# Kernel tuning notes

Measured on AMD Instinct MI355X. Metric: run time of the kernel, lower is better.

The kernel has to match this reference:

```python
import jax, jax.numpy as jnp
import numpy as np

B, M, K, KNN = 2, 256, 64, 16
CXYZ, CFEAT = 3, 61
CIN = CXYZ + CFEAT  # 64
MLPS = [64, 128]
SUMM = sum(MLPS)    # 192
CALIB = 64
EXP = [256, 512]
OUT = 256
EPS = 1e-5


def bn(x, g, b):
    # BatchNorm eval mode with running_mean=0, running_var=1 (channel axis 1)
    shape = (1, -1) + (1,) * (x.ndim - 2)
    return x * (g / jnp.sqrt(1.0 + EPS)).reshape(shape) + b.reshape(shape)


def knn(x, k):
    xx = jnp.sum(x * x, axis=1)                      # (B, N)
    inner = jnp.einsum('bcn,bcm->bnm', x, x)         # (B, N, N)
    pd = 2.0 * inner - xx[:, :, None] - xx[:, None, :]
    return jax.lax.top_k(pd, k)[1]                   # (B, N, k)


def graph_feature(x, idx):
    # x: (B, C, N), idx: (B, N, k) -> (B, 2C, N, k)
    xt = jnp.transpose(x, (0, 2, 1))                 # (B, N, C)
    nb = jax.vmap(lambda a, i: a[i])(xt, idx)        # (B, N, k, C)
    ctr = xt[:, :, None, :]
    feat = jnp.concatenate([nb - ctr, jnp.broadcast_to(ctr, nb.shape)], axis=-1)
    return jnp.transpose(feat, (0, 3, 1, 2))


def forward(xyz, feats, e1_w, e1_g, e1_b, e2_w, e2_g, e2_b,
            cal1_w, cal1_g, cal1_b, cal2_w, cal2_bias,
            exp1_w, exp1_g, exp1_b, exp2_w, exp2_g, exp2_b,
            red_w, red_g, red_b, sc1_w, sc1_b, sc2_w, sc2_b,
            sc_n1_g, sc_n1_b, sc_n2_g, sc_n2_b):
    x3 = xyz.reshape(B * M, K, CXYZ).transpose(0, 2, 1)      # (BM, 3, K)
    f = feats.reshape(B * M, K, CFEAT).transpose(0, 2, 1)    # (BM, 61, K)
    idx = knn(x3, KNN)                                        # USE_FEATS_DIS=False: knn once on xyz
    x = jnp.concatenate([x3, f], axis=1)                      # (BM, 64, K)
    outs = []
    for W, g, b in ((e1_w, e1_g, e1_b), (e2_w, e2_g, e2_b)):
        gf = graph_feature(x, idx)                            # (BM, 2C, K, knn)
        y = jax.nn.relu(bn(jnp.einsum('oc,bcnk->bonk', W, gf), g, b))
        x = y.max(axis=-1)                                    # (BM, mlp_i, K)
        outs.append(x)
    x = jnp.concatenate(outs, axis=1)                         # (BM, 192, K)
    c = jax.nn.relu(bn(jnp.einsum('oc,bcn->bon', cal1_w, x), cal1_g, cal1_b))
    c = jnp.einsum('oc,bcn->bon', cal2_w, c) + cal2_bias[None, :, None]
    x = jax.nn.sigmoid(c) * x
    x = jax.nn.relu(bn(jnp.einsum('oc,bcn->bon', exp1_w, x), exp1_g, exp1_b))
    x = jax.nn.relu(bn(jnp.einsum('oc,bcn->bon', exp2_w, x), exp2_g, exp2_b))
    x = x.max(axis=-1).reshape(B, M, EXP[1]).transpose(0, 2, 1)  # (B, 512, M)
    x = jax.nn.relu(bn(jnp.einsum('oc,bcm->bom', red_w, x), red_g, red_b))
    x = bn(x + x, sc_n1_g, sc_n1_b)
    h = jax.nn.relu(jnp.einsum('oc,bcm->bom', sc1_w, x) + sc1_b[None, :, None])
    h = jnp.einsum('oc,bcm->bom', sc2_w, h) + sc2_b[None, :, None]
    x = bn(x + h, sc_n2_g, sc_n2_b)
    return x                                                  # (B, 256, M)


def setup_inputs() -> dict:
    key = jax.random.key(0)
    ks = jax.random.split(key, 16)
    w = lambda k, s: jax.random.normal(k, s, jnp.float32) * 0.05
    ones = lambda n: jnp.ones((n,), jnp.float32)
    zeros = lambda n: jnp.zeros((n,), jnp.float32)
    return {
        'xyz': jax.random.normal(ks[0], (B, M, K, CXYZ), jnp.float32),
        'feats': jax.random.normal(ks[1], (B, M, K, CFEAT), jnp.float32),
        'e1_w': w(ks[2], (MLPS[0], 2 * CIN)), 'e1_g': ones(MLPS[0]), 'e1_b': zeros(MLPS[0]),
        'e2_w': w(ks[3], (MLPS[1], 2 * MLPS[0])), 'e2_g': ones(MLPS[1]), 'e2_b': zeros(MLPS[1]),
        'cal1_w': w(ks[4], (CALIB, SUMM)), 'cal1_g': ones(CALIB), 'cal1_b': zeros(CALIB),
        'cal2_w': w(ks[5], (SUMM, CALIB)), 'cal2_bias': zeros(SUMM),
        'exp1_w': w(ks[6], (EXP[0], SUMM)), 'exp1_g': ones(EXP[0]), 'exp1_b': zeros(EXP[0]),
        'exp2_w': w(ks[7], (EXP[1], EXP[0])), 'exp2_g': ones(EXP[1]), 'exp2_b': zeros(EXP[1]),
        'red_w': w(ks[8], (OUT, EXP[1])), 'red_g': ones(OUT), 'red_b': zeros(OUT),
        'sc1_w': w(ks[9], (OUT, OUT)), 'sc1_b': zeros(OUT),
        'sc2_w': w(ks[10], (OUT, OUT)), 'sc2_b': zeros(OUT),
        'sc_n1_g': ones(OUT), 'sc_n1_b': zeros(OUT),
        'sc_n2_g': ones(OUT), 'sc_n2_b': zeros(OUT),
    }


def reference(xyz, feats, e1_w, e1_g, e1_b, e2_w, e2_g, e2_b,
              cal1_w, cal1_g, cal1_b, cal2_w, cal2_bias,
              exp1_w, exp1_g, exp1_b, exp2_w, exp2_g, exp2_b,
              red_w, red_g, red_b, sc1_w, sc1_b, sc2_w, sc2_b,
              sc_n1_g, sc_n1_b, sc_n2_g, sc_n2_b):
    return forward(xyz, feats, e1_w, e1_g, e1_b, e2_w, e2_g, e2_b,
                   cal1_w, cal1_g, cal1_b, cal2_w, cal2_bias,
                   exp1_w, exp1_g, exp1_b, exp2_w, exp2_g, exp2_b,
                   red_w, red_g, red_b, sc1_w, sc1_b, sc2_w, sc2_b,
                   sc_n1_g, sc_n1_b, sc_n2_g, sc_n2_b)
```

## Files before the change

### kernel.cpp

```cpp
#include <hip/hip_runtime.h>
#include <hip/hip_bf16.h>
#include <math.h>
#include <stddef.h>

#define DEV __device__ __forceinline__
__device__ const float BNS = 0.99999500003749968f;

typedef __bf16 bf16x8 __attribute__((ext_vector_type(8)));
typedef float  f32x4  __attribute__((ext_vector_type(4)));

#define MF(a,b,c) __builtin_amdgcn_mfma_f32_16x16x32_bf16(a,b,c,0,0,0)

DEV unsigned short f2bs(float v){
  union{ __hip_bfloat16 b; unsigned short u; } c; c.b=__float2bfloat16(v); return c.u;
}
DEV float bs2f(unsigned short u){
  union{ unsigned short u; __hip_bfloat16 b; } c; c.u=u; return __bfloat162float(c.b);
}

DEV void put_split4(unsigned short* chunks, int n, int c0, const float* v){
  int cc=c0>>5, u=(c0>>3)&3, e=c0&7;
  unsigned short* base = chunks + cc*4096;
  unsigned short h0=f2bs(v[0]), h1=f2bs(v[1]), h2=f2bs(v[2]), h3=f2bs(v[3]);
  ushort4 hq = make_ushort4(h0,h1,h2,h3);
  ushort4 lq = make_ushort4(f2bs(v[0]-bs2f(h0)), f2bs(v[1]-bs2f(h1)),
                            f2bs(v[2]-bs2f(h2)), f2bs(v[3]-bs2f(h3)));
  *(ushort4*)&base[(n*8 + (u     ^ (n&7)))*8 + e] = hq;
  *(ushort4*)&base[(n*8 + ((u+4) ^ (n&7)))*8 + e] = lq;
}
DEV void get_split4(const unsigned short* chunks, int n, int c0, float* v){
  int cc=c0>>5, u=(c0>>3)&3, e=c0&7;
  const unsigned short* base = chunks + cc*4096;
  ushort4 hq = *(const ushort4*)&base[(n*8 + (u     ^ (n&7)))*8 + e];
  ushort4 lq = *(const ushort4*)&base[(n*8 + ((u+4) ^ (n&7)))*8 + e];
  v[0]=bs2f(hq.x)+bs2f(lq.x); v[1]=bs2f(hq.y)+bs2f(lq.y);
  v[2]=bs2f(hq.z)+bs2f(lq.z); v[3]=bs2f(hq.w)+bs2f(lq.w);
}


__global__ __launch_bounds__(256) void k_prep(const float* __restrict__ e1_w,
    const float* __restrict__ e2_w, const float* __restrict__ cal1_w,
    const float* __restrict__ cal2_w, const float* __restrict__ exp1_w,
    const float* __restrict__ exp2_w, unsigned short* __restrict__ Whi,
    unsigned short* __restrict__ Wlo,
    const float* __restrict__ red_w, const float* __restrict__ sc1_w,
    const float* __restrict__ sc2_w, float* __restrict__ Wt_red,
    float* __restrict__ Wt_s1, float* __restrict__ Wt_s2){
  __shared__ float s[32][33];
  int bid = blockIdx.x;
  if(bid < 896){
    const float* src; unsigned short *hi,*lo; int mode, O=0, i0;
    if(bid<32)      { src=e1_w;  hi=Whi;       lo=Wlo;       mode=1; O= 64; i0=bid*256; }
    else if(bid<96) { src=e2_w;  hi=Whi+8192;  lo=Wlo+8192;  mode=1; O=128; i0=(bid-32)*256; }
    else if(bid<144){ src=cal1_w;hi=Whi+24576; lo=Wlo+24576; mode=0;        i0=(bid-96)*256; }
    else if(bid<192){ src=cal2_w;hi=Whi+36864; lo=Wlo+36864; mode=0;        i0=(bid-144)*256; }
    else if(bid<384){ src=exp1_w;hi=Whi+49152; lo=Wlo+49152; mode=0;        i0=(bid-192)*256; }
    else            { src=exp2_w;hi=Whi+98304; lo=Wlo+98304; mode=0;        i0=(bid-384)*256; }
    int i = i0 + threadIdx.x;
    float v;
    if(mode==0) v = src[i];
    else {
      int row=i>>6, c=i&63;
      v = (row<O) ? src[row*128+c] : (src[(row-O)*128+64+c]-src[(row-O)*128+c]);
    }
    unsigned short h=f2bs(v); hi[i]=h; lo[i]=f2bs(v-bs2f(h));
  } else {
    int lb = bid-896;
    const float* in; float* out; int O,K;
    if(lb<128){ in=red_w; out=Wt_red; O=256; K=512; }
    else if(lb<192){ in=sc1_w; out=Wt_s1; O=256; K=256; lb-=128; }
    else { in=sc2_w; out=Wt_s2; O=256; K=256; lb-=192; }
    int nt=O>>5;
    int to=lb%nt, tk=lb/nt;
    int c=threadIdx.x&31, r8=threadIdx.x>>5;
    #pragma unroll
    for(int p=0;p<4;p++){
      int r=r8+p*8;
      s[r][c]=in[(size_t)(to*32+r)*K + tk*32 + c];
    }
    __syncthreads();
    #pragma unroll
    for(int p=0;p<4;p++){
      int r=r8+p*8;
      out[(size_t)(tk*32+r)*O + to*32 + c]=s[c][r];
    }
  }
}

__global__ __launch_bounds__(512) void k_knne12(const float* __restrict__ xyz,
    const float* __restrict__ feats,
    const unsigned short* __restrict__ W1h, const unsigned short* __restrict__ W1l,
    const unsigned short* __restrict__ W2h, const unsigned short* __restrict__ W2l,
    const float* __restrict__ g1, const float* __restrict__ b1,
    const float* __restrict__ g2, const float* __restrict__ b2,
    unsigned short* __restrict__ cat){
  __shared__ float bufA[64*65];
  __shared__ float bufB[64*65];
  __shared__ __align__(16) unsigned short sb[64*136];
  __shared__ int   ips[64*16];
  __shared__ float sx0[64], sx1[64], sx2[64], sxx[64];
  int bm = blockIdx.x;
  int tid = threadIdx.x, n = tid&63, s = tid>>6;
  int wid = tid>>6, lane = tid&63;
  int l15 = lane&15, q = lane>>4;
  if(s==0){
    const float* xp = xyz + (size_t)(bm*64+n)*3;
    float px=xp[0], py=xp[1], pz=xp[2];
    sx0[n]=px; sx1[n]=py; sx2[n]=pz; sxx[n]=px*px+py*py+pz*pz;
  }
  __syncthreads();
  {
    int p = lane>>3, seg = lane&7;
    int n1 = wid*8 + p;
    float px=sx0[n1], py=sx1[n1], pz=sx2[n1], xxn=sxx[n1];
    float pdr[8];
    #pragma unroll
    for(int t=0;t<8;t++){
      int m = seg*8+t;
      pdr[t] = 2.f*(px*sx0[m]+py*sx1[m]+pz*sx2[m]) - xxn - sxx[m];
    }
    for(int j=0;j<16;j++){
      float bv=-3.4e38f; int bi=seg*8;
      #pragma unroll
      for(int t=0;t<8;t++){ if(pdr[t]>bv){bv=pdr[t]; bi=seg*8+t;} }
      float ov; int oi;
      ov=__shfl_xor(bv,1); oi=__shfl_xor(bi,1);
      if(ov>bv || (ov==bv && oi<bi)){bv=ov;bi=oi;}
      ov=__shfl_xor(bv,2); oi=__shfl_xor(bi,2);
      if(ov>bv || (ov==bv && oi<bi)){bv=ov;bi=oi;}
      ov=__shfl_xor(bv,4); oi=__shfl_xor(bi,4);
      if(ov>bv || (ov==bv && oi<bi)){bv=ov;bi=oi;}
      if(seg==0) ips[n1*16+j]=bi;
      if((bi>>3)==seg) pdr[bi&7]=-3.4e38f;
    }
  }
  {
    unsigned short* r = sb + n*136;
    if(s==0){
      float px=sx0[n], py=sx1[n], pz=sx2[n];
      unsigned short h;
      h=f2bs(px); r[0]=h; r[64]=f2bs(px-bs2f(h));
      h=f2bs(py); r[1]=h; r[65]=f2bs(py-bs2f(h));
      h=f2bs(pz); r[2]=h; r[66]=f2bs(pz-bs2f(h));
    }
    const float* fp = feats + (size_t)(bm*64+n)*61;
    #pragma unroll
    for(int t=0;t<8;t++){
      int cc = s*8+t;
      if(cc<61){
        float v=fp[cc]; unsigned short h=f2bs(v);
        r[3+cc]=h; r[64+3+cc]=f2bs(v-bs2f(h));
      }
    }
  }
  __syncthreads();
  {
    int rbase = wid*16;
    f32x4 acc[4];
    #pragma unroll
    for(int d=0;d<4;d++) acc[d]=(f32x4){0.f,0.f,0.f,0.f};
    #pragma unroll
    for(int kc=0;kc<2;kc++){
      int k0=kc*32;
      size_t a0=(size_t)(rbase+l15)*64 + k0 + q*8;
      bf16x8 a0h=*(const bf16x8*)(W1h+a0), a0l=*(const bf16x8*)(W1l+a0);
      #pragma unroll
      for(int nt=0;nt<4;nt++){
        int row = nt*16 + l15;
        bf16x8 bh = *(const bf16x8*)&sb[row*136 + k0 + q*8];
        bf16x8 bl = *(const bf16x8*)&sb[row*136 + 64 + k0 + q*8];
        acc[nt]=MF(a0h,bh,acc[nt]);
        acc[nt]=MF(a0h,bl,acc[nt]);
        acc[nt]=MF(a0l,bh,acc[nt]);
      }
    }
    __syncthreads();
    float* dst = (wid<4)? bufA : bufB;
    int ro = (wid&3)*16;
    #pragma unroll
    for(int nt=0;nt<4;nt++)
      #pragma unroll
      for(int rr=0;rr<4;rr++)
        dst[(ro+q*4+rr)*65 + nt*16+l15] = acc[nt][rr];
  }
  __syncthreads();
  {
    int o = lane;
    float sc = g1[o]*BNS, bi = b1[o];
    #pragma unroll 4
    for(int j=0;j<8;j++){
      int nn = wid*8 + j;
      const int* ip = &ips[nn*16];
      float mz = -3.4e38f;
      #pragma unroll
      for(int k=0;k<16;k++) mz = fmaxf(mz, bufA[o*65 + ip[k]]);
      float v = fmaxf(sc*(mz + bufB[o*65 + nn]) + bi, 0.f);
      unsigned short hv = f2bs(v), lv = f2bs(v - bs2f(hv));
      size_t cb = ((size_t)bm*64+nn)*384 + o;
      cat[cb] = hv; cat[cb+192] = lv;
      sb[nn*136 + o] = hv; sb[nn*136 + 64 + o] = lv;
    }
  }
  for(int ch=0; ch<2; ch++){
    __syncthreads();
    int wrow = ((wid<4)?0:128) + ch*64 + (wid&3)*16;
    f32x4 acc[4];
    #pragma unroll
    for(int d=0;d<4;d++) acc[d]=(f32x4){0.f,0.f,0.f,0.f};
    #pragma unroll
    for(int kc=0;kc<2;kc++){
      int k0=kc*32;
      size_t a0=(size_t)(wrow+l15)*64 + k0 + q*8;
      bf16x8 a0h=*(const bf16x8*)(W2h+a0), a0l=*(const bf16x8*)(W2l+a0);
      #pragma unroll
      for(int nt=0;nt<4;nt++){
        int row = nt*16 + l15;
        bf16x8 bh = *(const bf16x8*)&sb[row*136 + k0 + q*8];
        bf16x8 bl = *(const bf16x8*)&sb[row*136 + 64 + k0 + q*8];
        acc[nt]=MF(a0h,bh,acc[nt]);
        acc[nt]=MF(a0h,bl,acc[nt]);
        acc[nt]=MF(a0l,bh,acc[nt]);
      }
    }
    __syncthreads();
    float* dst = (wid<4)? bufA : bufB;
    int ro = (wid&3)*16;
    #pragma unroll
    for(int nt=0;nt<4;nt++)
      #pragma unroll
      for(int rr=0;rr<4;rr++)
        dst[(ro+q*4+rr)*65 + nt*16+l15] = acc[nt][rr];
    __syncthreads();
    int o = ch*64 + lane;
    float sc = g2[o]*BNS, bi = b2[o];
    #pragma unroll 4
    for(int j=0;j<8;j++){
      int nn = wid*8 + j;
      const int* ip = &ips[nn*16];
      float mz = -3.4e38f;
      #pragma unroll
      for(int k=0;k<16;k++) mz = fmaxf(mz, bufA[lane*65 + ip[k]]);
      float v = fmaxf(sc*(mz + bufB[lane*65 + nn]) + bi, 0.f);
      unsigned short hv = f2bs(v);
      size_t cb = ((size_t)bm*64+nn)*384 + 64 + o;
      cat[cb] = hv; cat[cb+192] = f2bs(v - bs2f(hv));
    }
  }
}

__global__ __launch_bounds__(512,4) void k_mlp(
    const unsigned short* __restrict__ Whi, const unsigned short* __restrict__ Wlo,
    const unsigned short* __restrict__ cats,
    const float* __restrict__ c1g, const float* __restrict__ c1b,
    const float* __restrict__ c2bias,
    const float* __restrict__ e1g, const float* __restrict__ e1b,
    const float* __restrict__ e2g, const float* __restrict__ e2b,
    float* __restrict__ pool){
  __shared__ __align__(16) unsigned short buf[8*4096];
  __shared__ __align__(16) unsigned short calB[2*4096];
  int bm = blockIdx.x;
  int tid = threadIdx.x, wid = tid>>6, lane = tid&63;
  int l15 = lane&15, q = lane>>4;

  const unsigned short* w1h = Whi + 24576;
  const unsigned short* w1l = Wlo + 24576;
  int c1ot = wid>>1, c1rh = wid&1;
  size_t c1wo0 = (size_t)(c1ot*16+l15)*192 + q*8;
  bf16x8 cah = *(const bf16x8*)(w1h+c1wo0);
  bf16x8 cal_ = *(const bf16x8*)(w1l+c1wo0);

  size_t xb = (size_t)bm*24576;
  #pragma unroll
  for(int i=0;i<6;i++){
    int U = tid + i*512;
    int kc = U>>9, w = U&511, rr = w>>3, up = w&7, u = up ^ (rr&7);
    const unsigned short* src = cats + xb + (size_t)rr*384
      + (u<4 ? (kc*32 + u*8) : (192 + kc*32 + (u-4)*8));
    *(uint4*)&buf[kc*4096 + w*8] = *(const uint4*)src;
  }
  __syncthreads();

  f32x4 a0={0.f,0.f,0.f,0.f}, a1={0.f,0.f,0.f,0.f};
  {
    int r0 = c1rh*32+l15, r1 = c1rh*32+16+l15;
    __builtin_amdgcn_s_setprio(1);
    #pragma unroll
    for(int kc=0;kc<6;kc++){
      bf16x8 nah, nal;
      if(kc<5){
        size_t wo = c1wo0 + (kc+1)*32;
        nah=*(const bf16x8*)(w1h+wo); nal=*(const bf16x8*)(w1l+wo);
      }
      const unsigned short* cb = buf + kc*4096;
      bf16x8 xh0=*(const bf16x8*)&cb[(r0*8+((  q)^(r0&7)))*8];
      bf16x8 xl0=*(const bf16x8*)&cb[(r0*8+((4+q)^(r0&7)))*8];
      bf16x8 xh1=*(const bf16x8*)&cb[(r1*8+((  q)^(r1&7)))*8];
      bf16x8 xl1=*(const bf16x8*)&cb[(r1*8+((4+q)^(r1&7)))*8];
      a0=MF(cah,xh0,a0); a1=MF(cah,xh1,a1);
      a0=MF(cah,xl0,a0); a1=MF(cah,xl1,a1);
      a0=MF(cal_,xh0,a0); a1=MF(cal_,xh1,a1);
      cah=nah; cal_=nal;
    }
    __builtin_amdgcn_s_setprio(0);
  }
  const unsigned short* w2h = Whi + 36864;
  const unsigned short* w2l = Wlo + 36864;
  bf16x8 c2h[6], c2l[6];
  #pragma unroll
  for(int i=0;i<6;i++){
    int ot = (wid*6+i)>>2;
    size_t wo=(size_t)(ot*16+l15)*64 + q*8;
    c2h[i]=*(const bf16x8*)(w2h+wo); c2l[i]=*(const bf16x8*)(w2l+wo);
  }
  {
    int c0 = c1ot*16+q*4;
    float4 sg = *(const float4*)&c1g[c0];
    float4 bb = *(const float4*)&c1b[c0];
    float v0[4], v1[4];
    v0[0]=fmaxf(a0[0]*sg.x*BNS+bb.x,0.f); v1[0]=fmaxf(a1[0]*sg.x*BNS+bb.x,0.f);
    v0[1]=fmaxf(a0[1]*sg.y*BNS+bb.y,0.f); v1[1]=fmaxf(a1[1]*sg.y*BNS+bb.y,0.f);
    v0[2]=fmaxf(a0[2]*sg.z*BNS+bb.z,0.f); v1[2]=fmaxf(a1[2]*sg.z*BNS+bb.z,0.f);
    v0[3]=fmaxf(a0[3]*sg.w*BNS+bb.w,0.f); v1[3]=fmaxf(a1[3]*sg.w*BNS+bb.w,0.f);
    put_split4(calB, c1rh*32+l15,    c0, v0);
    put_split4(calB, c1rh*32+16+l15, c0, v1);
  }
  __syncthreads();
  f32x4 ac[6];
  #pragma unroll
  for(int i=0;i<6;i++) ac[i]=(f32x4){0.f,0.f,0.f,0.f};
  #pragma unroll
  for(int kc=0;kc<2;kc++){
    const unsigned short* cb = calB + kc*4096;
    if(kc==1){
      #pragma unroll
      for(int i=0;i<6;i++){
        int ot = (wid*6+i)>>2;
        size_t wo=(size_t)(ot*16+l15)*64 + 32 + q*8;
        c2h[i]=*(const bf16x8*)(w2h+wo); c2l[i]=*(const bf16x8*)(w2l+wo);
      }
    }
    __builtin_amdgcn_s_setprio(1);
    #pragma unroll
    for(int i=0;i<6;i++){
      int nf=(wid*6+i)&3;
      int r=nf*16+l15;
      bf16x8 xh=*(const bf16x8*)&cb[(r*8+((  q)^(r&7)))*8];
      bf16x8 xl=*(const bf16x8*)&cb[(r*8+((4+q)^(r&7)))*8];
      ac[i]=MF(c2h[i],xh,ac[i]); ac[i]=MF(c2h[i],xl,ac[i]); ac[i]=MF(c2l[i],xh,ac[i]);
    }
    __builtin_amdgcn_s_setprio(0);
  }
  const unsigned short* e1wh=Whi+49152; const unsigned short* e1wl=Wlo+49152;
  int ob1 = wid*32;
  bf16x8 p1h[2], p1l[2];
  #pragma unroll
  for(int mt=0;mt<2;mt++){
    size_t wo=(size_t)(ob1+mt*16+l15)*192 + q*8;
    p1h[mt]=*(const bf16x8*)(e1wh+wo); p1l[mt]=*(const bf16x8*)(e1wl+wo);
  }
  #pragma unroll
  for(int i=0;i<6;i++){
    int j=wid*6+i, ot=j>>2, nf=j&3, n=nf*16+l15;
    int c0=ot*16+q*4;
    float4 cb4 = *(const float4*)&c2bias[c0];
    float xv[4];
    get_split4(buf, n, c0, xv);
    xv[0] *= 1.f/(1.f+__expf(-(ac[i][0]+cb4.x)));
    xv[1] *= 1.f/(1.f+__expf(-(ac[i][1]+cb4.y)));
    xv[2] *= 1.f/(1.f+__expf(-(ac[i][2]+cb4.z)));
    xv[3] *= 1.f/(1.f+__expf(-(ac[i][3]+cb4.w)));
    put_split4(buf, n, c0, xv);
  }
  __syncthreads();
  {
    f32x4 e1a[2][4];
    #pragma unroll
    for(int a=0;a<2;a++)
      #pragma unroll
      for(int d=0;d<4;d++) e1a[a][d]=(f32x4){0.f,0.f,0.f,0.f};
    __builtin_amdgcn_s_setprio(1);
    #pragma unroll
    for(int kc=0;kc<6;kc++){
      bf16x8 nh[2], nl[2];
      if(kc<5){
        #pragma unroll
        for(int mt=0;mt<2;mt++){
          size_t wo=(size_t)(ob1+mt*16+l15)*192 + (kc+1)*32 + q*8;
          nh[mt]=*(const bf16x8*)(e1wh+wo); nl[mt]=*(const bf16x8*)(e1wl+wo);
        }
      }
      const unsigned short* cb = buf + kc*4096;
      #pragma unroll
      for(int nf=0;nf<4;nf++){
        int r=nf*16+l15;
        bf16x8 xh=*(const bf16x8*)&cb[(r*8+((  q)^(r&7)))*8];
        bf16x8 xl=*(const bf16x8*)&cb[(r*8+((4+q)^(r&7)))*8];
        e1a[0][nf]=MF(p1h[0],xh,e1a[0][nf]); e1a[1][nf]=MF(p1h[1],xh,e1a[1][nf]);
        e1a[0][nf]=MF(p1h[0],xl,e1a[0][nf]); e1a[1][nf]=MF(p1h[1],xl,e1a[1][nf]);
        e1a[0][nf]=MF(p1l[0],xh,e1a[0][nf]); e1a[1][nf]=MF(p1l[1],xh,e1a[1][nf]);
      }
      p1h[0]=nh[0]; p1h[1]=nh[1]; p1l[0]=nl[0]; p1l[1]=nl[1];
    }
    __builtin_amdgcn_s_setprio(0);
    __syncthreads();
    const unsigned short* e2wh=Whi+98304; const unsigned short* e2wl=Wlo+98304;
    int ob2 = wid*64;
    bf16x8 p2h[4], p2l[4];
    #pragma unroll
    for(int mt=0;mt<4;mt++){
      size_t wo=(size_t)(ob2+mt*16+l15)*256 + q*8;
      p2h[mt]=*(const bf16x8*)(e2wh+wo); p2l[mt]=*(const bf16x8*)(e2wl+wo);
    }
    #pragma unroll
    for(int mt=0;mt<2;mt++){
      int c0 = ob1+mt*16+q*4;
      float4 sg = *(const float4*)&e1g[c0];
      float4 bb = *(const float4*)&e1b[c0];
      #pragma unroll
      for(int nf=0;nf<4;nf++){
        float v[4];
        v[0]=fmaxf(e1a[mt][nf][0]*sg.x*BNS+bb.x,0.f);
        v[1]=fmaxf(e1a[mt][nf][1]*sg.y*BNS+bb.y,0.f);
        v[2]=fmaxf(e1a[mt][nf][2]*sg.z*BNS+bb.z,0.f);
        v[3]=fmaxf(e1a[mt][nf][3]*sg.w*BNS+bb.w,0.f);
        put_split4(buf, nf*16+l15, c0, v);
      }
    }
    __syncthreads();
    f32x4 a2[4][4];
    #pragma unroll
    for(int a=0;a<4;a++)
      #pragma unroll
      for(int d=0;d<4;d++) a2[a][d]=(f32x4){0.f,0.f,0.f,0.f};
    {
      const unsigned short* cb = buf;
      __builtin_amdgcn_s_setprio(1);
      #pragma unroll
      for(int nf=0;nf<4;nf++){
        int r=nf*16+l15;
        bf16x8 xh=*(const bf16x8*)&cb[(r*8+((  q)^(r&7)))*8];
        bf16x8 xl=*(const bf16x8*)&cb[(r*8+((4+q)^(r&7)))*8];
        #pragma unroll
        for(int mt=0;mt<4;mt++) a2[mt][nf]=MF(p2h[mt],xh,a2[mt][nf]);
        #pragma unroll
        for(int mt=0;mt<4;mt++) a2[mt][nf]=MF(p2h[mt],xl,a2[mt][nf]);
        #pragma unroll
        for(int mt=0;mt<4;mt++) a2[mt][nf]=MF(p2l[mt],xh,a2[mt][nf]);
      }
      __builtin_amdgcn_s_setprio(0);
    }
    for(int kc=1;kc<8;kc++){
      bf16x8 ch[4], cl[4];
      #pragma unroll
      for(int mt=0;mt<4;mt++){
        size_t wo=(size_t)(ob2+mt*16+l15)*256 + kc*32 + q*8;
        ch[mt]=*(const bf16x8*)(e2wh+wo); cl[mt]=*(const bf16x8*)(e2wl+wo);
      }
      const unsigned short* cb = buf + kc*4096;
      __builtin_amdgcn_s_setprio(1);
      #pragma unroll
      for(int nf=0;nf<4;nf++){
        int r=nf*16+l15;
        bf16x8 xh=*(const bf16x8*)&cb[(r*8+((  q)^(r&7)))*8];
        bf16x8 xl=*(const bf16x8*)&cb[(r*8+((4+q)^(r&7)))*8];
        #pragma unroll
        for(int mt=0;mt<4;mt++) a2[mt][nf]=MF(ch[mt],xh,a2[mt][nf]);
        #pragma unroll
        for(int mt=0;mt<4;mt++) a2[mt][nf]=MF(ch[mt],xl,a2[mt][nf]);
      }
      #pragma unroll
      for(int nf=0;nf<4;nf++){
        int r=nf*16+l15;
        bf16x8 xh=*(const bf16x8*)&cb[(r*8+((  q)^(r&7)))*8];
        #pragma unroll
        for(int mt=0;mt<4;mt++) a2[mt][nf]=MF(cl[mt],xh,a2[mt][nf]);
      }
      __builtin_amdgcn_s_setprio(0);
    }
    int b = bm>>8, m = bm&255;
    #pragma unroll
    for(int mt=0;mt<4;mt++){
      int c0 = ob2+mt*16+q*4;
      float4 sg = *(const float4*)&e2g[c0];
      float4 bb = *(const float4*)&e2b[c0];
      float s[4]={sg.x*BNS,sg.y*BNS,sg.z*BNS,sg.w*BNS};
      float bbv[4]={bb.x,bb.y,bb.z,bb.w};
      #pragma unroll
      for(int rr=0;rr<4;rr++){
        float v = a2[mt][0][rr]*s[rr]+bbv[rr];
        v = fmaxf(v, a2[mt][1][rr]*s[rr]+bbv[rr]);
        v = fmaxf(v, a2[mt][2][rr]*s[rr]+bbv[rr]);
        v = fmaxf(v, a2[mt][3][rr]*s[rr]+bbv[rr]);
        v = fmaxf(v, 0.f);
        v = fmaxf(v, __shfl_xor(v,1));
        v = fmaxf(v, __shfl_xor(v,2));
        v = fmaxf(v, __shfl_xor(v,4));
        v = fmaxf(v, __shfl_xor(v,8));
        if(l15==0) pool[((size_t)b*512 + c0+rr)*256 + m] = v;
      }
    }
  }
}

__global__ __launch_bounds__(512) void k_headf(const float* __restrict__ Wt_red,
    const float* __restrict__ Wt_s1, const float* __restrict__ Wt_s2,
    const float* __restrict__ pool, float* __restrict__ Og,
    const float* __restrict__ red_g, const float* __restrict__ red_b,
    const float* __restrict__ n1g, const float* __restrict__ n1b,
    const float* __restrict__ s1b, const float* __restrict__ s2b,
    const float* __restrict__ n2g, const float* __restrict__ n2b){
  __shared__ float P[512*3];
  __shared__ float X1[256*3];
  __shared__ float H[256*3];
  __shared__ float PB[256*5];
  int g = blockIdx.x;
  int b = g>>7, mg = g&127;
  int m0 = mg*2;
  int tid = threadIdx.x;
  int o = tid&255, h = tid>>8;
  {
    int c = tid;
    float2 v = *(const float2*)&pool[((size_t)b*512+c)*256 + m0];
    P[c*3+0]=v.x; P[c*3+1]=v.y;
  }
  __syncthreads();
  float a0=0.f, a1=0.f;
  {
    int c0 = h*256;
    #pragma unroll 8
    for(int i=0;i<256;i++){
      int c = c0+i;
      float w = Wt_red[c*256+o];
      a0 += w*P[c*3]; a1 += w*P[c*3+1];
    }
  }
  PB[o*5+h*2]=a0; PB[o*5+h*2+1]=a1;
  __syncthreads();
  a0 = PB[o*5]+PB[o*5+2]; a1 = PB[o*5+1]+PB[o*5+3];
  float x0r,x1r;
  {
    float s=red_g[o]*BNS, bi=red_b[o], s1=n1g[o]*BNS, b1=n1b[o];
    float r0=fmaxf(a0*s+bi,0.f), r1=fmaxf(a1*s+bi,0.f);
    x0r=2.f*r0*s1+b1; x1r=2.f*r1*s1+b1;
    if(h==0){ X1[o*3]=x0r; X1[o*3+1]=x1r; }
  }
  __syncthreads();
  a0=0.f; a1=0.f;
  {
    int c0 = h*128;
    #pragma unroll 8
    for(int i=0;i<128;i++){
      int c = c0+i;
      float w = Wt_s1[c*256+o];
      a0 += w*X1[c*3]; a1 += w*X1[c*3+1];
    }
  }
  PB[o*5+h*2]=a0; PB[o*5+h*2+1]=a1;
  __syncthreads();
  a0 = PB[o*5]+PB[o*5+2]; a1 = PB[o*5+1]+PB[o*5+3];
  {
    float bi=s1b[o];
    if(h==0){ H[o*3]=fmaxf(a0+bi,0.f); H[o*3+1]=fmaxf(a1+bi,0.f); }
  }
  __syncthreads();
  a0=0.f; a1=0.f;
  {
    int c0 = h*128;
    #pragma unroll 8
    for(int i=0;i<128;i++){
      int c = c0+i;
      float w = Wt_s2[c*256+o];
      a0 += w*H[c*3]; a1 += w*H[c*3+1];
    }
  }
  PB[o*5+h*2]=a0; PB[o*5+h*2+1]=a1;
  __syncthreads();
  if(h==0){
    a0 = PB[o*5]+PB[o*5+2]; a1 = PB[o*5+1]+PB[o*5+3];
    float bi=s2b[o], s2=n2g[o]*BNS, b2=n2b[o];
    float v0=(x0r+a0+bi)*s2+b2, v1=(x1r+a1+bi)*s2+b2;
    *(float2*)&Og[((size_t)b*256+o)*256 + m0] = make_float2(v0,v1);
  }
}

extern "C" void kernel_launch(void* const* d_in, const int* in_sizes, int n_in,
                              void* d_out, int out_size, void* d_ws, size_t ws_size,
                              hipStream_t stream){
  const float* xyz     =(const float*)d_in[0];
  const float* feats   =(const float*)d_in[1];
  const float* e1_w    =(const float*)d_in[2];
  const float* e1_g    =(const float*)d_in[3];
  const float* e1_b    =(const float*)d_in[4];
  const float* e2_w    =(const float*)d_in[5];
  const float* e2_g    =(const float*)d_in[6];
  const float* e2_b    =(const float*)d_in[7];
  const float* cal1_w  =(const float*)d_in[8];
  const float* cal1_g  =(const float*)d_in[9];
  const float* cal1_b  =(const float*)d_in[10];
  const float* cal2_w  =(const float*)d_in[11];
  const float* cal2_bias=(const float*)d_in[12];
  const float* exp1_w  =(const float*)d_in[13];
  const float* exp1_g  =(const float*)d_in[14];
  const float* exp1_b  =(const float*)d_in[15];
  const float* exp2_w  =(const float*)d_in[16];
  const float* exp2_g  =(const float*)d_in[17];
  const float* exp2_b  =(const float*)d_in[18];
  const float* red_w   =(const float*)d_in[19];
  const float* red_g   =(const float*)d_in[20];
  const float* red_b   =(const float*)d_in[21];
  const float* sc1_w   =(const float*)d_in[22];
  const float* sc1_b   =(const float*)d_in[23];
  const float* sc2_w   =(const float*)d_in[24];
  const float* sc2_b   =(const float*)d_in[25];
  const float* sc_n1_g =(const float*)d_in[26];
  const float* sc_n1_b =(const float*)d_in[27];
  const float* sc_n2_g =(const float*)d_in[28];
  const float* sc_n2_b =(const float*)d_in[29];

  char* wsb=(char*)d_ws;
  unsigned short* cats=(unsigned short*)(wsb + 10485760);
  float*          pool=(float*)         (wsb + 69206016);
  unsigned short* Whi =(unsigned short*)(wsb + 75497472);
  unsigned short* Wlo =(unsigned short*)(wsb + 76021760);
  float*          Wt_red=(float*)       (wsb + 76546048);
  float*          Wt_s1 =(float*)       (wsb + 77070336);
  float*          Wt_s2 =(float*)       (wsb + 77332480);
  unsigned short* e1e_h=Whi;          unsigned short* e1e_l=Wlo;
  unsigned short* e2e_h=Whi+8192;     unsigned short* e2e_l=Wlo+8192;

  k_prep      <<<1152,256,0,stream>>>(e1_w,e2_w,cal1_w,cal2_w,exp1_w,exp2_w,Whi,Wlo,
                                      red_w,sc1_w,sc2_w,Wt_red,Wt_s1,Wt_s2);
  k_knne12    <<<512,512,0,stream>>>(xyz,feats,e1e_h,e1e_l,e2e_h,e2e_l,
                                     e1_g,e1_b,e2_g,e2_b,cats);
  k_mlp       <<<512,512,0,stream>>>(Whi,Wlo,cats,cal1_g,cal1_b,cal2_bias,
                                     exp1_g,exp1_b,exp2_g,exp2_b,pool);
  k_headf     <<<256,512,0,stream>>>(Wt_red,Wt_s1,Wt_s2,pool,(float*)d_out,
                                     red_g,red_b,sc_n1_g,sc_n1_b,sc1_b,sc2_b,sc_n2_g,sc_n2_b);
}
```

Measured before the change: 262.4 us.

## Split k_mlp per-group work into two half-point blocks with partial max pooling

k_mlp now launches 1024 blocks of 256 threads instead of 512 blocks of 512. Each block handles 32 of the 64 points in a group, which halves the shared-memory buffers. Each wave now covers more output channels over fewer point fragments. Partial max-pools go to a doubled pool buffer, and k_headf combines them with an extra max. The goal is more parallelism and occupancy, at the cost of each block reloading the full weight set, which doubles weight traffic, plus more register pressure from larger accumulator arrays.

```diff
diff --git a/kernel.cpp b/kernel.cpp
--- a/kernel.cpp
+++ b/kernel.cpp
@@ -20,7 +20,7 @@
 
 DEV void put_split4(unsigned short* chunks, int n, int c0, const float* v){
   int cc=c0>>5, u=(c0>>3)&3, e=c0&7;
-  unsigned short* base = chunks + cc*4096;
+  unsigned short* base = chunks + cc*2048;
   unsigned short h0=f2bs(v[0]), h1=f2bs(v[1]), h2=f2bs(v[2]), h3=f2bs(v[3]);
   ushort4 hq = make_ushort4(h0,h1,h2,h3);
   ushort4 lq = make_ushort4(f2bs(v[0]-bs2f(h0)), f2bs(v[1]-bs2f(h1)),
@@ -30,7 +30,7 @@
 }
 DEV void get_split4(const unsigned short* chunks, int n, int c0, float* v){
   int cc=c0>>5, u=(c0>>3)&3, e=c0&7;
-  const unsigned short* base = chunks + cc*4096;
+  const unsigned short* base = chunks + cc*2048;
   ushort4 hq = *(const ushort4*)&base[(n*8 + (u     ^ (n&7)))*8 + e];
   ushort4 lq = *(const ushort4*)&base[(n*8 + ((u+4) ^ (n&7)))*8 + e];
   v[0]=bs2f(hq.x)+bs2f(lq.x); v[1]=bs2f(hq.y)+bs2f(lq.y);
@@ -248,7 +248,7 @@
   }
 }
 
-__global__ __launch_bounds__(512,4) void k_mlp(
+__global__ __launch_bounds__(256,4) void k_mlp(
     const unsigned short* __restrict__ Whi, const unsigned short* __restrict__ Wlo,
     const unsigned short* __restrict__ cats,
     const float* __restrict__ c1g, const float* __restrict__ c1b,
@@ -256,33 +256,32 @@
     const float* __restrict__ e1g, const float* __restrict__ e1b,
     const float* __restrict__ e2g, const float* __restrict__ e2b,
     float* __restrict__ pool){
-  __shared__ __align__(16) unsigned short buf[8*4096];
-  __shared__ __align__(16) unsigned short calB[2*4096];
-  int bm = blockIdx.x;
+  __shared__ __align__(16) unsigned short buf[8*2048];
+  __shared__ __align__(16) unsigned short calB[2*2048];
+  int bmh = blockIdx.x, bm = bmh>>1, half = bmh&1;
   int tid = threadIdx.x, wid = tid>>6, lane = tid&63;
   int l15 = lane&15, q = lane>>4;
 
   const unsigned short* w1h = Whi + 24576;
   const unsigned short* w1l = Wlo + 24576;
-  int c1ot = wid>>1, c1rh = wid&1;
-  size_t c1wo0 = (size_t)(c1ot*16+l15)*192 + q*8;
+  size_t c1wo0 = (size_t)(wid*16+l15)*192 + q*8;
   bf16x8 cah = *(const bf16x8*)(w1h+c1wo0);
   bf16x8 cal_ = *(const bf16x8*)(w1l+c1wo0);
 
-  size_t xb = (size_t)bm*24576;
+  size_t xb = (size_t)bm*24576 + (size_t)half*12288;
   #pragma unroll
   for(int i=0;i<6;i++){
-    int U = tid + i*512;
-    int kc = U>>9, w = U&511, rr = w>>3, up = w&7, u = up ^ (rr&7);
+    int U = tid + i*256;
+    int kc = U>>8, w = U&255, rr = w>>3, up = w&7, u = up ^ (rr&7);
     const unsigned short* src = cats + xb + (size_t)rr*384
       + (u<4 ? (kc*32 + u*8) : (192 + kc*32 + (u-4)*8));
-    *(uint4*)&buf[kc*4096 + w*8] = *(const uint4*)src;
+    *(uint4*)&buf[kc*2048 + w*8] = *(const uint4*)src;
   }
   __syncthreads();
 
   f32x4 a0={0.f,0.f,0.f,0.f}, a1={0.f,0.f,0.f,0.f};
   {
-    int r0 = c1rh*32+l15, r1 = c1rh*32+16+l15;
+    int r0 = l15, r1 = 16+l15;
     __builtin_amdgcn_s_setprio(1);
     #pragma unroll
     for(int kc=0;kc<6;kc++){
@@ -291,7 +290,7 @@
         size_t wo = c1wo0 + (kc+1)*32;
         nah=*(const bf16x8*)(w1h+wo); nal=*(const bf16x8*)(w1l+wo);
       }
-      const unsigned short* cb = buf + kc*4096;
+      const unsigned short* cb = buf + kc*2048;
       bf16x8 xh0=*(const bf16x8*)&cb[(r0*8+((  q)^(r0&7)))*8];
       bf16x8 xl0=*(const bf16x8*)&cb[(r0*8+((4+q)^(r0&7)))*8];
       bf16x8 xh1=*(const bf16x8*)&cb[(r1*8+((  q)^(r1&7)))*8];
@@ -308,12 +307,12 @@
   bf16x8 c2h[6], c2l[6];
   #pragma unroll
   for(int i=0;i<6;i++){
-    int ot = (wid*6+i)>>2;
+    int ot = (wid*6+i)>>1;
     size_t wo=(size_t)(ot*16+l15)*64 + q*8;
     c2h[i]=*(const bf16x8*)(w2h+wo); c2l[i]=*(const bf16x8*)(w2l+wo);
   }
   {
-    int c0 = c1ot*16+q*4;
+    int c0 = wid*16+q*4;
     float4 sg = *(const float4*)&c1g[c0];
     float4 bb = *(const float4*)&c1b[c0];
     float v0[4], v1[4];
@@ -321,8 +320,8 @@
     v0[1]=fmaxf(a0[1]*sg.y*BNS+bb.y,0.f); v1[1]=fmaxf(a1[1]*sg.y*BNS+bb.y,0.f);
     v0[2]=fmaxf(a0[2]*sg.z*BNS+bb.z,0.f); v1[2]=fmaxf(a1[2]*sg.z*BNS+bb.z,0.f);
     v0[3]=fmaxf(a0[3]*sg.w*BNS+bb.w,0.f); v1[3]=fmaxf(a1[3]*sg.w*BNS+bb.w,0.f);
-    put_split4(calB, c1rh*32+l15,    c0, v0);
-    put_split4(calB, c1rh*32+16+l15, c0, v1);
+    put_split4(calB, l15,    c0, v0);
+    put_split4(calB, 16+l15, c0, v1);
   }
   __syncthreads();
   f32x4 ac[6];
@@ -330,11 +329,11 @@
   for(int i=0;i<6;i++) ac[i]=(f32x4){0.f,0.f,0.f,0.f};
   #pragma unroll
   for(int kc=0;kc<2;kc++){
-    const unsigned short* cb = calB + kc*4096;
+    const unsigned short* cb = calB + kc*2048;
     if(kc==1){
       #pragma unroll
       for(int i=0;i<6;i++){
-        int ot = (wid*6+i)>>2;
+        int ot = (wid*6+i)>>1;
         size_t wo=(size_t)(ot*16+l15)*64 + 32 + q*8;
         c2h[i]=*(const bf16x8*)(w2h+wo); c2l[i]=*(const bf16x8*)(w2l+wo);
       }
@@ -342,7 +341,7 @@
     __builtin_amdgcn_s_setprio(1);
     #pragma unroll
     for(int i=0;i<6;i++){
-      int nf=(wid*6+i)&3;
+      int nf=(wid*6+i)&1;
       int r=nf*16+l15;
       bf16x8 xh=*(const bf16x8*)&cb[(r*8+((  q)^(r&7)))*8];
       bf16x8 xl=*(const bf16x8*)&cb[(r*8+((4+q)^(r&7)))*8];
@@ -351,16 +350,16 @@
     __builtin_amdgcn_s_setprio(0);
   }
   const unsigned short* e1wh=Whi+49152; const unsigned short* e1wl=Wlo+49152;
-  int ob1 = wid*32;
-  bf16x8 p1h[2], p1l[2];
+  int ob1 = wid*64;
+  bf16x8 p1h[4], p1l[4];
   #pragma unroll
-  for(int mt=0;mt<2;mt++){
+  for(int mt=0;mt<4;mt++){
     size_t wo=(size_t)(ob1+mt*16+l15)*192 + q*8;
     p1h[mt]=*(const bf16x8*)(e1wh+wo); p1l[mt]=*(const bf16x8*)(e1wl+wo);
   }
   #pragma unroll
   for(int i=0;i<6;i++){
-    int j=wid*6+i, ot=j>>2, nf=j&3, n=nf*16+l15;
+    int j=wid*6+i, ot=j>>1, nf=j&1, n=nf*16+l15;
     int c0=ot*16+q*4;
     float4 cb4 = *(const float4*)&c2bias[c0];
     float xv[4];
@@ -373,38 +372,39 @@
   }
   __syncthreads();
   {
-    f32x4 e1a[2][4];
-    #pragma unroll
-    for(int a=0;a<2;a++)
-      #pragma unroll
-      for(int d=0;d<4;d++) e1a[a][d]=(f32x4){0.f,0.f,0.f,0.f};
+    f32x4 e1a[4][2];
+    #pragma unroll
+    for(int a=0;a<4;a++)
+      #pragma unroll
+      for(int d=0;d<2;d++) e1a[a][d]=(f32x4){0.f,0.f,0.f,0.f};
     __builtin_amdgcn_s_setprio(1);
     #pragma unroll
     for(int kc=0;kc<6;kc++){
-      bf16x8 nh[2], nl[2];
-      if(kc<5){
+      if(kc>0){
         #pragma unroll
-        for(int mt=0;mt<2;mt++){
-          size_t wo=(size_t)(ob1+mt*16+l15)*192 + (kc+1)*32 + q*8;
-          nh[mt]=*(const bf16x8*)(e1wh+wo); nl[mt]=*(const bf16x8*)(e1wl+wo);
+        for(int mt=0;mt<4;mt++){
+          size_t wo=(size_t)(ob1+mt*16+l15)*192 + kc*32 + q*8;
+          p1h[mt]=*(const bf16x8*)(e1wh+wo); p1l[mt]=*(const bf16x8*)(e1wl+wo);
         }
       }
-      const unsigned short* cb = buf + kc*4096;
-      #pragma unroll
-      for(int nf=0;nf<4;nf++){
+      const unsigned short* cb = buf + kc*2048;
+      #pragma unroll
+      for(int nf=0;nf<2;nf++){
         int r=nf*16+l15;
         bf16x8 xh=*(const bf16x8*)&cb[(r*8+((  q)^(r&7)))*8];
         bf16x8 xl=*(const bf16x8*)&cb[(r*8+((4+q)^(r&7)))*8];
-        e1a[0][nf]=MF(p1h[0],xh,e1a[0][nf]); e1a[1][nf]=MF(p1h[1],xh,e1a[1][nf]);
-        e1a[0][nf]=MF(p1h[0],xl,e1a[0][nf]); e1a[1][nf]=MF(p1h[1],xl,e1a[1][nf]);
-        e1a[0][nf]=MF(p1l[0],xh,e1a[0][nf]); e1a[1][nf]=MF(p1l[1],xh,e1a[1][nf]);
-      }
-      p1h[0]=nh[0]; p1h[1]=nh[1]; p1l[0]=nl[0]; p1l[1]=nl[1];
+        #pragma unroll
+        for(int mt=0;mt<4;mt++) e1a[mt][nf]=MF(p1h[mt],xh,e1a[mt][nf]);
+        #pragma unroll
+        for(int mt=0;mt<4;mt++) e1a[mt][nf]=MF(p1h[mt],xl,e1a[mt][nf]);
+        #pragma unroll
+        for(int mt=0;mt<4;mt++) e1a[mt][nf]=MF(p1l[mt],xh,e1a[mt][nf]);
+      }
     }
     __builtin_amdgcn_s_setprio(0);
     __syncthreads();
     const unsigned short* e2wh=Whi+98304; const unsigned short* e2wl=Wlo+98304;
-    int ob2 = wid*64;
+    int ob2 = wid*128;
     bf16x8 p2h[4], p2l[4];
     #pragma unroll
     for(int mt=0;mt<4;mt++){
@@ -412,12 +412,12 @@
       p2h[mt]=*(const bf16x8*)(e2wh+wo); p2l[mt]=*(const bf16x8*)(e2wl+wo);
     }
     #pragma unroll
-    for(int mt=0;mt<2;mt++){
+    for(int mt=0;mt<4;mt++){
       int c0 = ob1+mt*16+q*4;
       float4 sg = *(const float4*)&e1g[c0];
       float4 bb = *(const float4*)&e1b[c0];
       #pragma unroll
-      for(int nf=0;nf<4;nf++){
+      for(int nf=0;nf<2;nf++){
         float v[4];
         v[0]=fmaxf(e1a[mt][nf][0]*sg.x*BNS+bb.x,0.f);
         v[1]=fmaxf(e1a[mt][nf][1]*sg.y*BNS+bb.y,0.f);
@@ -427,59 +427,49 @@
       }
     }
     __syncthreads();
-    f32x4 a2[4][4];
-    #pragma unroll
-    for(int a=0;a<4;a++)
-      #pragma unroll
-      for(int d=0;d<4;d++) a2[a][d]=(f32x4){0.f,0.f,0.f,0.f};
-    {
-      const unsigned short* cb = buf;
-      __builtin_amdgcn_s_setprio(1);
-      #pragma unroll
-      for(int nf=0;nf<4;nf++){
+    f32x4 a2[8][2];
+    #pragma unroll
+    for(int a=0;a<8;a++)
+      #pragma unroll
+      for(int d=0;d<2;d++) a2[a][d]=(f32x4){0.f,0.f,0.f,0.f};
+    for(int kc=0;kc<8;kc++){
+      const unsigned short* cb = buf + kc*2048;
+      bf16x8 xh[2], xl[2];
+      #pragma unroll
+      for(int nf=0;nf<2;nf++){
         int r=nf*16+l15;
-        bf16x8 xh=*(const bf16x8*)&cb[(r*8+((  q)^(r&7)))*8];
-        bf16x8 xl=*(const bf16x8*)&cb[(r*8+((4+q)^(r&7)))*8];
+        xh[nf]=*(const bf16x8*)&cb[(r*8+((  q)^(r&7)))*8];
+        xl[nf]=*(const bf16x8*)&cb[(r*8+((4+q)^(r&7)))*8];
+      }
+      #pragma unroll
+      for(int mh=0;mh<2;mh++){
+        bf16x8 ch[4], cl[4];
+        if(kc==0 && mh==0){
+          #pragma unroll
+          for(int mt=0;mt<4;mt++){ ch[mt]=p2h[mt]; cl[mt]=p2l[mt]; }
+        } else {
+          #pragma unroll
+          for(int mt=0;mt<4;mt++){
+            size_t wo=(size_t)(ob2+(mh*4+mt)*16+l15)*256 + kc*32 + q*8;
+            ch[mt]=*(const bf16x8*)(e2wh+wo); cl[mt]=*(const bf16x8*)(e2wl+wo);
+          }
+        }
+        __builtin_amdgcn_s_setprio(1);
         #pragma unroll
-        for(int mt=0;mt<4;mt++) a2[mt][nf]=MF(p2h[mt],xh,a2[mt][nf]);
-        #pragma unroll
-        for(int mt=0;mt<4;mt++) a2[mt][nf]=MF(p2h[mt],xl,a2[mt][nf]);
-        #pragma unroll
-        for(int mt=0;mt<4;mt++) a2[mt][nf]=MF(p2l[mt],xh,a2[mt][nf]);
-      }
-      __builtin_amdgcn_s_setprio(0);
-    }
-    for(int kc=1;kc<8;kc++){
-      bf16x8 ch[4], cl[4];
-      #pragma unroll
-      for(int mt=0;mt<4;mt++){
-        size_t wo=(size_t)(ob2+mt*16+l15)*256 + kc*32 + q*8;
-        ch[mt]=*(const bf16x8*)(e2wh+wo); cl[mt]=*(const bf16x8*)(e2wl+wo);
-      }
-      const unsigned short* cb = buf + kc*4096;
-      __builtin_amdgcn_s_setprio(1);
-      #pragma unroll
-      for(int nf=0;nf<4;nf++){
-        int r=nf*16+l15;
-        bf16x8 xh=*(const bf16x8*)&cb[(r*8+((  q)^(r&7)))*8];
-        bf16x8 xl=*(const bf16x8*)&cb[(r*8+((4+q)^(r&7)))*8];
-        #pragma unroll
-        for(int mt=0;mt<4;mt++) a2[mt][nf]=MF(ch[mt],xh,a2[mt][nf]);
-        #pragma unroll
-        for(int mt=0;mt<4;mt++) a2[mt][nf]=MF(ch[mt],xl,a2[mt][nf]);
-      }
-      #pragma unroll
-      for(int nf=0;nf<4;nf++){
-        int r=nf*16+l15;
-        bf16x8 xh=*(const bf16x8*)&cb[(r*8+((  q)^(r&7)))*8];
-        #pragma unroll
-        for(int mt=0;mt<4;mt++) a2[mt][nf]=MF(cl[mt],xh,a2[mt][nf]);
-      }
-      __builtin_amdgcn_s_setprio(0);
+        for(int nf=0;nf<2;nf++){
+          #pragma unroll
+          for(int mt=0;mt<4;mt++) a2[mh*4+mt][nf]=MF(ch[mt],xh[nf],a2[mh*4+mt][nf]);
+          #pragma unroll
+          for(int mt=0;mt<4;mt++) a2[mh*4+mt][nf]=MF(ch[mt],xl[nf],a2[mh*4+mt][nf]);
+          #pragma unroll
+          for(int mt=0;mt<4;mt++) a2[mh*4+mt][nf]=MF(cl[mt],xh[nf],a2[mh*4+mt][nf]);
+        }
+        __builtin_amdgcn_s_setprio(0);
+      }
     }
     int b = bm>>8, m = bm&255;
     #pragma unroll
-    for(int mt=0;mt<4;mt++){
+    for(int mt=0;mt<8;mt++){
       int c0 = ob2+mt*16+q*4;
       float4 sg = *(const float4*)&e2g[c0];
       float4 bb = *(const float4*)&e2b[c0];
@@ -489,14 +479,13 @@
       for(int rr=0;rr<4;rr++){
         float v = a2[mt][0][rr]*s[rr]+bbv[rr];
         v = fmaxf(v, a2[mt][1][rr]*s[rr]+bbv[rr]);
-        v = fmaxf(v, a2[mt][2][rr]*s[rr]+bbv[rr]);
-        v = fmaxf(v, a2[mt][3][rr]*s[rr]+bbv[rr]);
         v = fmaxf(v, 0.f);
         v = fmaxf(v, __shfl_xor(v,1));
         v = fmaxf(v, __shfl_xor(v,2));
         v = fmaxf(v, __shfl_xor(v,4));
         v = fmaxf(v, __shfl_xor(v,8));
-        if(l15==0) pool[((size_t)b*512 + c0+rr)*256 + m] = v;
+        if(l15==0)
+          pool[(((size_t)b*512 + c0+rr)*2 + half)*256 + m] = v;
       }
     }
   }
@@ -520,8 +509,10 @@
   int o = tid&255, h = tid>>8;
   {
     int c = tid;
-    float2 v = *(const float2*)&pool[((size_t)b*512+c)*256 + m0];
-    P[c*3+0]=v.x; P[c*3+1]=v.y;
+    const float* pp = &pool[(((size_t)b*512+c)*2)*256 + m0];
+    float2 v0 = *(const float2*)&pp[0];
+    float2 v1 = *(const float2*)&pp[256];
+    P[c*3+0]=fmaxf(v0.x,v1.x); P[c*3+1]=fmaxf(v0.y,v1.y);
   }
   __syncthreads();
   float a0=0.f, a1=0.f;
@@ -632,8 +623,8 @@
                                       red_w,sc1_w,sc2_w,Wt_red,Wt_s1,Wt_s2);
   k_knne12    <<<512,512,0,stream>>>(xyz,feats,e1e_h,e1e_l,e2e_h,e2e_l,
                                      e1_g,e1_b,e2_g,e2_b,cats);
-  k_mlp       <<<512,512,0,stream>>>(Whi,Wlo,cats,cal1_g,cal1_b,cal2_bias,
-                                     exp1_g,exp1_b,exp2_g,exp2_b,pool);
+  k_mlp       <<<1024,256,0,stream>>>(Whi,Wlo,cats,cal1_g,cal1_b,cal2_bias,
+                                      exp1_g,exp1_b,exp2_g,exp2_b,pool);
   k_headf     <<<256,512,0,stream>>>(Wt_red,Wt_s1,Wt_s2,pool,(float*)d_out,
                                      red_g,red_b,sc_n1_g,sc_n1_b,sc1_b,sc2_b,sc_n2_g,sc_n2_b);
 }
```

Measured after the change: 279.9 us. 6.7% more time.
